# Kernel optimization log

Measured on AMD Instinct MI355X. Metric: run time of the kernel, lower is better.

## Reference

```python
import math
import jax, jax.numpy as jnp
import numpy as np

D = 1536      # d_model
H = 12        # n_heads
L = 12        # n_layers
V = 50257     # vocab (hardcoded in module)
P = 1024      # max positions (hardcoded)
B = 1         # batch (must be 1: pos-embed uses arange(len(idx)))
S = 1024      # sequence length


def setup_inputs() -> dict:
    key = jax.random.key(0)
    ks = jax.random.split(key, 10)
    sc = 0.02
    n = lambda k, shape: (jax.random.normal(k, shape, jnp.float32) * sc)
    return {
        "idx": jax.random.randint(ks[0], (B, S), 0, V),
        "mask": jnp.tril(jnp.ones((S, S), jnp.int32)),  # causal mask
        "tok_emb": n(ks[1], (V, D)),
        "pos_emb": n(ks[2], (P, D)),
        "Wqkv": n(ks[3], (L, D, 3 * D)), "bqkv": jnp.zeros((L, 3 * D), jnp.float32),
        "Wo":   n(ks[4], (L, D, D)),     "bo":   jnp.zeros((L, D), jnp.float32),
        "W1":   n(ks[5], (L, D, 4 * D)), "b1":   jnp.zeros((L, 4 * D), jnp.float32),
        "W2":   n(ks[6], (L, 4 * D, D)), "b2":   jnp.zeros((L, D), jnp.float32),
        "ln_g": jnp.ones((D,), jnp.float32), "ln_b": jnp.zeros((D,), jnp.float32),
        "Wout": n(ks[7], (D, D)), "bout": jnp.zeros((D,), jnp.float32),
    }


def _gpt_forward(idx, mask, tok_emb, pos_emb, Wqkv, bqkv, Wo, bo,
                 W1, b1, W2, b2, ln_g, ln_b, Wout, bout):
    b, s = idx.shape
    d = tok_emb.shape[1]
    hd = d // H
    scale = 1.0 / math.sqrt(d)  # note: module divides by sqrt(d_model), not head_dim

    # faithful quirk: position_embedding(arange(len(idx))) -> (B, D), broadcasts since B==1
    x = tok_emb[idx] + pos_emb[:b]  # (B,S,D)

    mask0 = (mask == 0)  # (S,S) -> broadcast over (B,H,S,S)

    def block(x, p):
        wqkv, bqkv_, wo, bo_, w1, b1_, w2, b2_ = p
        qkv = x @ wqkv + bqkv_                       # (B,S,3D)
        q, k, v = jnp.split(qkv, 3, axis=-1)
        q = q.reshape(b, s, H, hd)
        k = k.reshape(b, s, H, hd)
        v = v.reshape(b, s, H, hd)
        scores = jnp.einsum('bqhd,bkhd->bhqk', q, k) * scale
        scores = jnp.where(mask0, -jnp.inf, scores)
        attn = jax.nn.softmax(scores, axis=-2)       # non-standard: softmax over QUERY axis
        o = jnp.einsum('bhqk,bkhd->bqhd', attn, v).reshape(b, s, d)
        x = x + (o @ wo + bo_)                       # attention residual
        x = x + (jax.nn.relu(x @ w1 + b1_) @ w2 + b2_)  # FFN residual (on post-attn x)
        return x, None

    x, _ = jax.lax.scan(block, x, (Wqkv, bqkv, Wo, bo, W1, b1, W2, b2))

    # final LayerNorm (eps=1e-5 like torch default)
    mu = jnp.mean(x, axis=-1, keepdims=True)
    var = jnp.mean(jnp.square(x - mu), axis=-1, keepdims=True)
    xn = (x - mu) * jax.lax.rsqrt(var + 1e-5) * ln_g + ln_b
    return xn @ Wout + bout


def reference(idx, mask, tok_emb, pos_emb, Wqkv, bqkv, Wo, bo,
              W1, b1, W2, b2, ln_g, ln_b, Wout, bout):
    return _gpt_forward(idx, mask, tok_emb, pos_emb, Wqkv, bqkv, Wo, bo,
                        W1, b1, W2, b2, ln_g, ln_b, Wout, bout)
```

## Files before the change

kernel.cpp:

```cpp
#include <hip/hip_runtime.h>
#include <stdint.h>
#include <math.h>

#define D_MODEL 1536
#define NH 12
#define HD 128
#define NL 12
#define SEQ 1024
#define D3 4608
#define D4 6144
#define SCALE 0.025515518153991442f

typedef __attribute__((ext_vector_type(8))) short short8;
typedef __attribute__((ext_vector_type(4))) float floatx4;

__device__ __forceinline__ uint32_t packhi(float a, float b) {
  return (__float_as_uint(a) >> 16) | (__float_as_uint(b) & 0xFFFF0000u);
}
__device__ __forceinline__ float truncf32(float a) {
  return __uint_as_float(__float_as_uint(a) & 0xFFFF0000u);
}
__device__ __forceinline__ void split8v(float4 v0, float4 v1, uint4 &hi, uint4 &lo) {
  hi.x = packhi(v0.x, v0.y); hi.y = packhi(v0.z, v0.w);
  hi.z = packhi(v1.x, v1.y); hi.w = packhi(v1.z, v1.w);
  lo.x = packhi(v0.x - truncf32(v0.x), v0.y - truncf32(v0.y));
  lo.y = packhi(v0.z - truncf32(v0.z), v0.w - truncf32(v0.w));
  lo.z = packhi(v1.x - truncf32(v1.x), v1.y - truncf32(v1.y));
  lo.w = packhi(v1.z - truncf32(v1.z), v1.w - truncf32(v1.w));
}

__device__ __forceinline__ int xcd_chunk_id(int nwg) {
  int orig = blockIdx.x;
  int xcd = orig & 7, pos = orig >> 3;
  int q = nwg >> 3, r = nwg & 7;
  return (xcd < r ? xcd * (q + 1) : r * (q + 1) + (xcd - r) * q) + pos;
}

__global__ __launch_bounds__(256)
void embed_kernel(const int* __restrict__ idx, const float* __restrict__ tok,
                  const float* __restrict__ pos, float* __restrict__ x) {
  int i = blockIdx.x * 256 + threadIdx.x;
  int s = i / D_MODEL;
  int d = i - s * D_MODEL;
  x[i] = tok[(size_t)idx[s] * D_MODEL + d] + pos[d];
}

template<int BM, bool RELU, bool RES, int SPLITK, bool TA2>
__global__ __launch_bounds__(256)
void mgemm_kernel(const float* __restrict__ A, const float* __restrict__ Ab,
                  const float* __restrict__ B,
                  const float* __restrict__ bias, const float* __restrict__ res,
                  float* __restrict__ C, int M, int N, int K, int NC, int NR) {
  constexpr int MI = BM / 32;
  constexpr int AE = BM / 8;
  constexpr int TPR = 32 / AE;
  __shared__ short Ah[2][BM][36], Al[2][BM][36];
  __shared__ short Bh[2][128][36], Bl[2][128][36];
  const int tid = threadIdx.x;
  const int lane = tid & 63, wave = tid >> 6;

  const int lid = xcd_chunk_id(NC * NR * SPLITK);
  const int z   = lid / (NC * NR);
  const int rem = lid - z * (NC * NR);
  const int ct  = rem / NR;
  const int rt  = rem - ct * NR;
  const int bm = rt * BM, bn = ct << 7;

  const int wm = (wave >> 1) * (BM / 2), wn = (wave & 1) << 6;
  const int fr = lane & 15, fk = (lane >> 4) << 3;
  const int Kc = K / SPLITK;
  const int kbase = (SPLITK > 1) ? z * Kc : 0;

  floatx4 acc[MI][4];
#pragma unroll
  for (int i = 0; i < MI; i++)
#pragma unroll
    for (int j = 0; j < 4; j++) acc[i][j] = (floatx4){0.f, 0.f, 0.f, 0.f};

  const int ar = tid / TPR;
  const int ac = (tid % TPR) * AE;
  const int bc = tid & 127;
  const int bkq = (tid >> 7) << 4;
  const float* Ag  = A + (size_t)(bm + ar) * K + kbase + ac;
  const float* Ag2 = TA2 ? (Ab + (size_t)(bm + ar) * K + kbase + ac) : nullptr;
  const float* Bg = B + (size_t)(kbase + bkq) * N + bn + bc;

  float a_reg[AE];
  float b_reg[16];

  auto LOADG = [&](int k0) {
#pragma unroll
    for (int e = 0; e < AE / 4; e++) {
      float4 v = *(const float4*)(Ag + k0 + 4 * e);
      if constexpr (TA2) {
        float4 w = *(const float4*)(Ag2 + k0 + 4 * e);
        v.x += w.x; v.y += w.y; v.z += w.z; v.w += w.w;
      }
      a_reg[4 * e + 0] = v.x; a_reg[4 * e + 1] = v.y;
      a_reg[4 * e + 2] = v.z; a_reg[4 * e + 3] = v.w;
    }
    const float* Bp = Bg + (size_t)k0 * N;
#pragma unroll
    for (int j = 0; j < 16; j++) b_reg[j] = Bp[(size_t)j * N];
  };
  auto STORE = [&](int buf) {
#pragma unroll
    for (int e = 0; e < AE / 8; e++) {
      float4 v0 = {a_reg[8 * e + 0], a_reg[8 * e + 1], a_reg[8 * e + 2], a_reg[8 * e + 3]};
      float4 v1 = {a_reg[8 * e + 4], a_reg[8 * e + 5], a_reg[8 * e + 6], a_reg[8 * e + 7]};
      uint4 hi, lo; split8v(v0, v1, hi, lo);
      *(uint4*)&Ah[buf][ar][ac + 8 * e] = hi;
      *(uint4*)&Al[buf][ar][ac + 8 * e] = lo;
    }
#pragma unroll
    for (int e = 0; e < 2; e++) {
      float4 u0 = {b_reg[8 * e + 0], b_reg[8 * e + 1], b_reg[8 * e + 2], b_reg[8 * e + 3]};
      float4 u1 = {b_reg[8 * e + 4], b_reg[8 * e + 5], b_reg[8 * e + 6], b_reg[8 * e + 7]};
      uint4 hi, lo; split8v(u0, u1, hi, lo);
      *(uint4*)&Bh[buf][bc][bkq + 8 * e] = hi;
      *(uint4*)&Bl[buf][bc][bkq + 8 * e] = lo;
    }
  };

  LOADG(0);
  STORE(0);
  __syncthreads();

  for (int k0 = 0; k0 < Kc; k0 += 32) {
    const int cur = (k0 >> 5) & 1;
    const bool more = (k0 + 32 < Kc);
    if (more) LOADG(k0 + 32);

    short8 ah[MI], al[MI], bh[4], bl[4];
#pragma unroll
    for (int i = 0; i < MI; i++) {
      ah[i] = *(const short8*)&Ah[cur][wm + (i << 4) + fr][fk];
      al[i] = *(const short8*)&Al[cur][wm + (i << 4) + fr][fk];
    }
#pragma unroll
    for (int j = 0; j < 4; j++) {
      bh[j] = *(const short8*)&Bh[cur][wn + (j << 4) + fr][fk];
      bl[j] = *(const short8*)&Bl[cur][wn + (j << 4) + fr][fk];
    }
#pragma unroll
    for (int i = 0; i < MI; i++)
#pragma unroll
      for (int j = 0; j < 4; j++) {
        acc[i][j] = __builtin_amdgcn_mfma_f32_16x16x32_bf16(ah[i], bh[j], acc[i][j], 0, 0, 0);
        acc[i][j] = __builtin_amdgcn_mfma_f32_16x16x32_bf16(ah[i], bl[j], acc[i][j], 0, 0, 0);
        acc[i][j] = __builtin_amdgcn_mfma_f32_16x16x32_bf16(al[i], bh[j], acc[i][j], 0, 0, 0);
      }

    if (more) STORE(cur ^ 1);
    __syncthreads();
  }

  const int cr = (lane >> 4) << 2, cc = lane & 15;
  if constexpr (SPLITK > 1) {
    float* Cp = C + (size_t)z * M * N;
#pragma unroll
    for (int j = 0; j < 4; j++) {
      const int col = bn + wn + (j << 4) + cc;
#pragma unroll
      for (int i = 0; i < MI; i++) {
        const int row0 = bm + wm + (i << 4) + cr;
#pragma unroll
        for (int r = 0; r < 4; r++)
          Cp[(size_t)(row0 + r) * N + col] = acc[i][j][r];
      }
    }
  } else {
#pragma unroll
    for (int j = 0; j < 4; j++) {
      const int col = bn + wn + (j << 4) + cc;
      const float bv = bias[col];
#pragma unroll
      for (int i = 0; i < MI; i++) {
        const int row0 = bm + wm + (i << 4) + cr;
#pragma unroll
        for (int r = 0; r < 4; r++) {
          float v = acc[i][j][r] + bv;
          if constexpr (RES) v += res[(size_t)(row0 + r) * N + col];
          if constexpr (RELU) v = fmaxf(v, 0.f);
          C[(size_t)(row0 + r) * N + col] = v;
        }
      }
    }
  }
}

template<bool HASB, bool RES, bool RELU>
__global__ __launch_bounds__(256)
void combine_kernel(const float* __restrict__ p0, const float* __restrict__ p1,
                    const float* __restrict__ bias, const float* __restrict__ res,
                    float* __restrict__ C, int N) {
  const int i = (blockIdx.x * 256 + threadIdx.x) << 2;
  float4 a = *(const float4*)&p0[i];
  float4 b = *(const float4*)&p1[i];
  float4 r = {a.x + b.x, a.y + b.y, a.z + b.z, a.w + b.w};
  if constexpr (HASB) {
    const int col = i % N;
    float4 bv = *(const float4*)&bias[col];
    r.x += bv.x; r.y += bv.y; r.z += bv.z; r.w += bv.w;
  }
  if constexpr (RES) {
    float4 rv = *(const float4*)&res[i];
    r.x += rv.x; r.y += rv.y; r.z += rv.z; r.w += rv.w;
  }
  if constexpr (RELU) {
    r.x = fmaxf(r.x, 0.f); r.y = fmaxf(r.y, 0.f);
    r.z = fmaxf(r.z, 0.f); r.w = fmaxf(r.w, 0.f);
  }
  *(float4*)&C[i] = r;
}

__global__ __launch_bounds__(256)
void scores_kernel(const float* __restrict__ qkv, float* __restrict__ scores,
                   float* __restrict__ pstats) {
  __shared__ short Qh[128][40], Ql[128][40], Kh[128][40], Kl[128][40];
  const int tid = threadIdx.x;
  const int lane = tid & 63, wave = tid >> 6;

  const int lid = xcd_chunk_id(NH * 36);
  const int h = lid / 36;
  int t = lid - h * 36;
  int rr = 0;
  while ((rr + 1) * (rr + 2) / 2 <= t) rr++;
  const int bi = rr << 7;
  const int bj = (t - rr * (rr + 1) / 2) << 7;

  const int wm = (wave >> 1) << 6, wn = (wave & 1) << 6;
  const int fr = lane & 15, fk = (lane >> 4) << 3;
  const float* Q = qkv + h * HD;
  const float* Kp = qkv + D_MODEL + h * HD;

  floatx4 acc[4][4];
#pragma unroll
  for (int i = 0; i < 4; i++)
#pragma unroll
    for (int j = 0; j < 4; j++) acc[i][j] = (floatx4){0.f, 0.f, 0.f, 0.f};

  const int ar = tid >> 1;
  const int ac = (tid & 1) << 4;

  for (int k0 = 0; k0 < HD; k0 += 32) {
    __syncthreads();
    {
      const float* Qp = Q + (size_t)(bi + ar) * D3 + k0 + ac;
#pragma unroll
      for (int e = 0; e < 2; e++) {
        float4 v0 = *(const float4*)(Qp + 8 * e);
        float4 v1 = *(const float4*)(Qp + 8 * e + 4);
        uint4 hi, lo; split8v(v0, v1, hi, lo);
        *(uint4*)&Qh[ar][ac + 8 * e] = hi;
        *(uint4*)&Ql[ar][ac + 8 * e] = lo;
      }
      const float* Kpp = Kp + (size_t)(bj + ar) * D3 + k0 + ac;
#pragma unroll
      for (int e = 0; e < 2; e++) {
        float4 v0 = *(const float4*)(Kpp + 8 * e);
        float4 v1 = *(const float4*)(Kpp + 8 * e + 4);
        uint4 hi, lo; split8v(v0, v1, hi, lo);
        *(uint4*)&Kh[ar][ac + 8 * e] = hi;
        *(uint4*)&Kl[ar][ac + 8 * e] = lo;
      }
    }
    __syncthreads();
    short8 qh[4], ql[4], kh[4], kl[4];
#pragma unroll
    for (int i = 0; i < 4; i++) {
      qh[i] = *(const short8*)&Qh[wm + (i << 4) + fr][fk];
      ql[i] = *(const short8*)&Ql[wm + (i << 4) + fr][fk];
      kh[i] = *(const short8*)&Kh[wn + (i << 4) + fr][fk];
      kl[i] = *(const short8*)&Kl[wn + (i << 4) + fr][fk];
    }
#pragma unroll
    for (int i = 0; i < 4; i++)
#pragma unroll
      for (int j = 0; j < 4; j++) {
        acc[i][j] = __builtin_amdgcn_mfma_f32_16x16x32_bf16(qh[i], kh[j], acc[i][j], 0, 0, 0);
        acc[i][j] = __builtin_amdgcn_mfma_f32_16x16x32_bf16(qh[i], kl[j], acc[i][j], 0, 0, 0);
        acc[i][j] = __builtin_amdgcn_mfma_f32_16x16x32_bf16(ql[i], kh[j], acc[i][j], 0, 0, 0);
        acc[i][j] = __builtin_amdgcn_mfma_f32_16x16x32_bf16(ql[i], kl[j], acc[i][j], 0, 0, 0);
      }
  }

  const int cr = (lane >> 4) << 2, cc = lane & 15;
  float* S = scores + (size_t)h * SEQ * SEQ;
  const int qc = (bi >> 6) + (wave >> 1);
  float* Pm = pstats + (size_t)((h * 16 + qc) * 2 + 0) * 1024;
  float* Pz = pstats + (size_t)((h * 16 + qc) * 2 + 1) * 1024;
#pragma unroll
  for (int j = 0; j < 4; j++) {
    const int col = bj + wn + (j << 4) + cc;
    float vv[16];
    float m = -1e30f;
#pragma unroll
    for (int i = 0; i < 4; i++) {
      const int row0 = bi + wm + (i << 4) + cr;
#pragma unroll
      for (int r = 0; r < 4; r++) {
        float v = (col <= row0 + r) ? acc[i][j][r] * SCALE : -1e30f;
        S[(size_t)(row0 + r) * SEQ + col] = v;
        vv[i * 4 + r] = v;
        m = fmaxf(m, v);
      }
    }
    float zz = 0.f;
#pragma unroll
    for (int t2 = 0; t2 < 16; t2++) zz += __expf(vv[t2] - m);
    if (m == -1e30f) zz = 0.f;
#pragma unroll
    for (int off = 16; off <= 32; off <<= 1) {
      float mo = __shfl_xor(m, off, 64);
      float zo = __shfl_xor(zz, off, 64);
      float mn = fmaxf(m, mo);
      zz = zz * __expf(m - mn) + zo * __expf(mo - mn);
      m = mn;
    }
    if ((lane >> 4) == 0) { Pm[col] = m; Pz[col] = zz; }
  }
}

__global__ __launch_bounds__(256)
void av_kernel(const float* __restrict__ qkv, const float* __restrict__ scores,
               const float* __restrict__ pstats, float* __restrict__ part) {
  __shared__ short Ph[64][40], Pl[64][40], Vh[128][40], Vl[128][40];
  __shared__ float Ms[512], Rs[512];
  const int tid = threadIdx.x;
  const int lane = tid & 63, wave = tid >> 6;

  const int lid = xcd_chunk_id(NH * 32);
  const int h = lid >> 5;
  const int t = lid & 31;
  const int y = t >> 1, z = t & 1;
  const int bm = y << 6;

  const int wm = (wave >> 1) << 5, wn = (wave & 1) << 6;
  const int fr = lane & 15, fk = (lane >> 4) << 3;
  const float* S = scores + (size_t)h * SEQ * SEQ;
  const float* V = qkv + 2 * D_MODEL + h * HD;

  const int kbeg = z * (y + 1) * 32;
  const int kend = (z + 1) * (y + 1) * 32;
  const int ncols = kend - kbeg;

  for (int c0 = tid; c0 < ncols; c0 += 256) {
    const int c = kbeg + c0;
    const int q0 = c >> 6;
    float m = -1e30f;
    for (int qc = q0; qc < 16; qc++)
      m = fmaxf(m, pstats[(size_t)((h * 16 + qc) * 2 + 0) * 1024 + c]);
    float zz = 0.f;
    for (int qc = q0; qc < 16; qc++) {
      float pm = pstats[(size_t)((h * 16 + qc) * 2 + 0) * 1024 + c];
      float pz = pstats[(size_t)((h * 16 + qc) * 2 + 1) * 1024 + c];
      zz += pz * __expf(pm - m);
    }
    Ms[c0] = m;
    Rs[c0] = 1.f / zz;
  }

  floatx4 acc[2][4];
#pragma unroll
  for (int i = 0; i < 2; i++)
#pragma unroll
    for (int j = 0; j < 4; j++) acc[i][j] = (floatx4){0.f, 0.f, 0.f, 0.f};

  const int ar = tid >> 2;
  const int ac = (tid & 3) << 3;
  const int bc = tid & 127;
  const int bkq = (tid >> 7) << 4;

  for (int k0 = kbeg; k0 < kend; k0 += 32) {
    __syncthreads();
    {
      const float* Sp = S + (size_t)(bm + ar) * SEQ + k0 + ac;
      float4 v0 = *(const float4*)(Sp);
      float4 v1 = *(const float4*)(Sp + 4);
      float t8[8] = {v0.x, v0.y, v0.z, v0.w, v1.x, v1.y, v1.z, v1.w};
      float4 p0, p1;
      {
        int kk = k0 - kbeg + ac;
        p0.x = __expf(t8[0] - Ms[kk + 0]) * Rs[kk + 0];
        p0.y = __expf(t8[1] - Ms[kk + 1]) * Rs[kk + 1];
        p0.z = __expf(t8[2] - Ms[kk + 2]) * Rs[kk + 2];
        p0.w = __expf(t8[3] - Ms[kk + 3]) * Rs[kk + 3];
        p1.x = __expf(t8[4] - Ms[kk + 4]) * Rs[kk + 4];
        p1.y = __expf(t8[5] - Ms[kk + 5]) * Rs[kk + 5];
        p1.z = __expf(t8[6] - Ms[kk + 6]) * Rs[kk + 6];
        p1.w = __expf(t8[7] - Ms[kk + 7]) * Rs[kk + 7];
      }
      uint4 hi, lo; split8v(p0, p1, hi, lo);
      *(uint4*)&Ph[ar][ac] = hi;
      *(uint4*)&Pl[ar][ac] = lo;
    }
    {
      const float* Vp = V + (size_t)(k0 + bkq) * D3 + bc;
#pragma unroll
      for (int e = 0; e < 2; e++) {
        float4 u0, u1;
        u0.x = Vp[(size_t)(8 * e + 0) * D3]; u0.y = Vp[(size_t)(8 * e + 1) * D3];
        u0.z = Vp[(size_t)(8 * e + 2) * D3]; u0.w = Vp[(size_t)(8 * e + 3) * D3];
        u1.x = Vp[(size_t)(8 * e + 4) * D3]; u1.y = Vp[(size_t)(8 * e + 5) * D3];
        u1.z = Vp[(size_t)(8 * e + 6) * D3]; u1.w = Vp[(size_t)(8 * e + 7) * D3];
        uint4 hi, lo; split8v(u0, u1, hi, lo);
        *(uint4*)&Vh[bc][bkq + 8 * e] = hi;
        *(uint4*)&Vl[bc][bkq + 8 * e] = lo;
      }
    }
    __syncthreads();
    short8 ph[2], pl[2], vh[4], vl[4];
#pragma unroll
    for (int i = 0; i < 2; i++) {
      ph[i] = *(const short8*)&Ph[wm + (i << 4) + fr][fk];
      pl[i] = *(const short8*)&Pl[wm + (i << 4) + fr][fk];
    }
#pragma unroll
    for (int j = 0; j < 4; j++) {
      vh[j] = *(const short8*)&Vh[wn + (j << 4) + fr][fk];
      vl[j] = *(const short8*)&Vl[wn + (j << 4) + fr][fk];
    }
#pragma unroll
    for (int i = 0; i < 2; i++)
#pragma unroll
      for (int j = 0; j < 4; j++) {
        acc[i][j] = __builtin_amdgcn_mfma_f32_16x16x32_bf16(ph[i], vh[j], acc[i][j], 0, 0, 0);
        acc[i][j] = __builtin_amdgcn_mfma_f32_16x16x32_bf16(ph[i], vl[j], acc[i][j], 0, 0, 0);
        acc[i][j] = __builtin_amdgcn_mfma_f32_16x16x32_bf16(pl[i], vh[j], acc[i][j], 0, 0, 0);
      }
  }

  const int cr = (lane >> 4) << 2, cc = lane & 15;
  float* Cp = part + (size_t)z * SEQ * D_MODEL;
#pragma unroll
  for (int j = 0; j < 4; j++) {
    const int col = h * HD + wn + (j << 4) + cc;
#pragma unroll
    for (int i = 0; i < 2; i++) {
      const int row0 = bm + wm + (i << 4) + cr;
#pragma unroll
      for (int r = 0; r < 4; r++)
        Cp[(size_t)(row0 + r) * D_MODEL + col] = acc[i][j][r];
    }
  }
}

__global__ __launch_bounds__(256)
void ln_kernel(const float* __restrict__ x, const float* __restrict__ g,
               const float* __restrict__ bb, float* __restrict__ y) {
  __shared__ float red[8];
  const int row = blockIdx.x;
  const float* xr = x + (size_t)row * D_MODEL;
  float v[6];
  float s = 0.f, sq = 0.f;
#pragma unroll
  for (int i = 0; i < 6; i++) {
    v[i] = xr[256 * i + threadIdx.x];
    s += v[i];
    sq += v[i] * v[i];
  }
#pragma unroll
  for (int off = 32; off >= 1; off >>= 1) {
    s += __shfl_down(s, off, 64);
    sq += __shfl_down(sq, off, 64);
  }
  const int lane = threadIdx.x & 63, w = threadIdx.x >> 6;
  if (lane == 0) { red[w] = s; red[4 + w] = sq; }
  __syncthreads();
  if (threadIdx.x == 0) {
    red[0] = red[0] + red[1] + red[2] + red[3];
    red[4] = red[4] + red[5] + red[6] + red[7];
  }
  __syncthreads();
  const float mu = red[0] * (1.f / D_MODEL);
  const float var = red[4] * (1.f / D_MODEL) - mu * mu;
  const float rs = rsqrtf(var + 1e-5f);
#pragma unroll
  for (int i = 0; i < 6; i++) {
    int c = 256 * i + threadIdx.x;
    y[(size_t)row * D_MODEL + c] = (v[i] - mu) * rs * g[c] + bb[c];
  }
}

extern "C" void kernel_launch(void* const* d_in, const int* in_sizes, int n_in,
                              void* d_out, int out_size, void* d_ws, size_t ws_size,
                              hipStream_t stream) {
  (void)in_sizes; (void)n_in; (void)out_size; (void)ws_size;
  const int*   idx     = (const int*)d_in[0];
  const float* tok_emb = (const float*)d_in[2];
  const float* pos_emb = (const float*)d_in[3];
  const float* Wqkv    = (const float*)d_in[4];
  const float* bqkv    = (const float*)d_in[5];
  const float* Wo      = (const float*)d_in[6];
  const float* bo      = (const float*)d_in[7];
  const float* W1      = (const float*)d_in[8];
  const float* b1      = (const float*)d_in[9];
  const float* W2      = (const float*)d_in[10];
  const float* b2      = (const float*)d_in[11];
  const float* ln_g    = (const float*)d_in[12];
  const float* ln_b    = (const float*)d_in[13];
  const float* Wout    = (const float*)d_in[14];
  const float* bout    = (const float*)d_in[15];
  float* out = (float*)d_out;

  char* ws = (char*)d_ws;
  float* x      = (float*)(ws);
  float* qkv    = (float*)(ws + 6291456);
  float* pstats = (float*)(ws + 25165824);
  float* part   = (float*)(ws + 26836992);
  float* U      = (float*)(ws + 52002816);
  float* scores = U;
  float* h1     = U;
  float* xn     = U;
  const size_t PN = (size_t)SEQ * D_MODEL;

  embed_kernel<<<6144, 256, 0, stream>>>(idx, tok_emb, pos_emb, x);

  for (int l = 0; l < NL; l++) {
    const float* wqkv = Wqkv + (size_t)l * D_MODEL * D3;
    const float* bq   = bqkv + (size_t)l * D3;
    const float* wo   = Wo   + (size_t)l * D_MODEL * D_MODEL;
    const float* bo_  = bo   + (size_t)l * D_MODEL;
    const float* w1   = W1   + (size_t)l * D_MODEL * D4;
    const float* b1_  = b1   + (size_t)l * D4;
    const float* w2   = W2   + (size_t)l * D4 * D_MODEL;
    const float* b2_  = b2   + (size_t)l * D_MODEL;

    mgemm_kernel<128, false, false, 1, false><<<288, 256, 0, stream>>>(
        x, nullptr, wqkv, bq, nullptr, qkv, SEQ, D3, D_MODEL, 36, 8);
    scores_kernel<<<432, 256, 0, stream>>>(qkv, scores, pstats);
    av_kernel<<<384, 256, 0, stream>>>(qkv, scores, pstats, part);
    mgemm_kernel<64, false, false, 2, true><<<384, 256, 0, stream>>>(
        part, part + PN, wo, nullptr, nullptr, part + 2 * PN,
        SEQ, D_MODEL, D_MODEL, 12, 16);
    combine_kernel<true, true, false><<<1536, 256, 0, stream>>>(
        part + 2 * PN, part + 3 * PN, bo_, x, x, D_MODEL);
    mgemm_kernel<128, true, false, 1, false><<<384, 256, 0, stream>>>(
        x, nullptr, w1, b1_, nullptr, h1, SEQ, D4, D_MODEL, 48, 8);
    mgemm_kernel<64, false, false, 2, false><<<384, 256, 0, stream>>>(
        h1, nullptr, w2, nullptr, nullptr, part, SEQ, D_MODEL, D4, 12, 16);
    combine_kernel<true, true, false><<<1536, 256, 0, stream>>>(
        part, part + PN, b2_, x, x, D_MODEL);
  }

  ln_kernel<<<SEQ, 256, 0, stream>>>(x, ln_g, ln_b, xn);
  mgemm_kernel<64, false, false, 2, false><<<384, 256, 0, stream>>>(
      xn, nullptr, Wout, nullptr, nullptr, part, SEQ, D_MODEL, D_MODEL, 12, 16);
  combine_kernel<true, false, false><<<1536, 256, 0, stream>>>(
      part, part + PN, bout, nullptr, out, D_MODEL);
}
```

Measured before the change: 5.060 ms.

## Fuse whole forward pass into a persistent cooperative megakernel with grid syncs

Replaces roughly a hundred separate kernel launches with one cooperative persistent kernel that loops over work items for each stage and uses grid-wide syncs between stages. The goal is to remove launch overhead and inter-kernel gaps. To fit a shared smem buffer and two blocks per CU, the GEMM drops its register/LDS double buffering and syncs twice per k-step, which may cost GEMM throughput. Fixed grid size (up to 768 blocks) means stages with more work items than blocks run in multiple passes. A fallback path keeps the old multi-kernel sequence.

```diff
diff --git a/kernel.cpp b/kernel.cpp
--- a/kernel.cpp
+++ b/kernel.cpp
@@ -1,6 +1,9 @@
 #include <hip/hip_runtime.h>
+#include <hip/hip_cooperative_groups.h>
 #include <stdint.h>
 #include <math.h>
+
+namespace cg = cooperative_groups;
 
 #define D_MODEL 1536
 #define NH 12
@@ -29,37 +32,39 @@
   lo.w = packhi(v1.z - truncf32(v1.z), v1.w - truncf32(v1.w));
 }
 
-__device__ __forceinline__ int xcd_chunk_id(int nwg) {
-  int orig = blockIdx.x;
+__device__ __forceinline__ int xcd_chunk(int orig, int nwg) {
   int xcd = orig & 7, pos = orig >> 3;
   int q = nwg >> 3, r = nwg & 7;
   return (xcd < r ? xcd * (q + 1) : r * (q + 1) + (xcd - r) * q) + pos;
 }
 
-__global__ __launch_bounds__(256)
-void embed_kernel(const int* __restrict__ idx, const float* __restrict__ tok,
-                  const float* __restrict__ pos, float* __restrict__ x) {
-  int i = blockIdx.x * 256 + threadIdx.x;
+__device__ __forceinline__ void d_embed(int wi, const int* __restrict__ idx,
+                                        const float* __restrict__ tok,
+                                        const float* __restrict__ pos,
+                                        float* __restrict__ x) {
+  int i = wi * 256 + threadIdx.x;
   int s = i / D_MODEL;
   int d = i - s * D_MODEL;
   x[i] = tok[(size_t)idx[s] * D_MODEL + d] + pos[d];
 }
 
 template<int BM, bool RELU, bool RES, int SPLITK, bool TA2>
-__global__ __launch_bounds__(256)
-void mgemm_kernel(const float* __restrict__ A, const float* __restrict__ Ab,
-                  const float* __restrict__ B,
-                  const float* __restrict__ bias, const float* __restrict__ res,
-                  float* __restrict__ C, int M, int N, int K, int NC, int NR) {
+__device__ void d_mgemm(char* smem, int orig,
+                        const float* __restrict__ A, const float* __restrict__ Ab,
+                        const float* __restrict__ B,
+                        const float* __restrict__ bias, const float* __restrict__ res,
+                        float* __restrict__ C, int M, int N, int K, int NC, int NR) {
   constexpr int MI = BM / 32;
   constexpr int AE = BM / 8;
   constexpr int TPR = 32 / AE;
-  __shared__ short Ah[2][BM][36], Al[2][BM][36];
-  __shared__ short Bh[2][128][36], Bl[2][128][36];
+  short* AhS = (short*)smem;
+  short* AlS = AhS + BM * 36;
+  short* BhS = AlS + BM * 36;
+  short* BlS = BhS + 128 * 36;
   const int tid = threadIdx.x;
   const int lane = tid & 63, wave = tid >> 6;
 
-  const int lid = xcd_chunk_id(NC * NR * SPLITK);
+  const int lid = xcd_chunk(orig, NC * NR * SPLITK);
   const int z   = lid / (NC * NR);
   const int rem = lid - z * (NC * NR);
   const int ct  = rem / NR;
@@ -88,7 +93,7 @@
   float a_reg[AE];
   float b_reg[16];
 
-  auto LOADG = [&](int k0) {
+  for (int k0 = 0; k0 < Kc; k0 += 32) {
 #pragma unroll
     for (int e = 0; e < AE / 4; e++) {
       float4 v = *(const float4*)(Ag + k0 + 4 * e);
@@ -99,48 +104,40 @@
       a_reg[4 * e + 0] = v.x; a_reg[4 * e + 1] = v.y;
       a_reg[4 * e + 2] = v.z; a_reg[4 * e + 3] = v.w;
     }
-    const float* Bp = Bg + (size_t)k0 * N;
-#pragma unroll
-    for (int j = 0; j < 16; j++) b_reg[j] = Bp[(size_t)j * N];
-  };
-  auto STORE = [&](int buf) {
+    {
+      const float* Bp = Bg + (size_t)k0 * N;
+#pragma unroll
+      for (int j = 0; j < 16; j++) b_reg[j] = Bp[(size_t)j * N];
+    }
+    __syncthreads();
 #pragma unroll
     for (int e = 0; e < AE / 8; e++) {
       float4 v0 = {a_reg[8 * e + 0], a_reg[8 * e + 1], a_reg[8 * e + 2], a_reg[8 * e + 3]};
       float4 v1 = {a_reg[8 * e + 4], a_reg[8 * e + 5], a_reg[8 * e + 6], a_reg[8 * e + 7]};
       uint4 hi, lo; split8v(v0, v1, hi, lo);
-      *(uint4*)&Ah[buf][ar][ac + 8 * e] = hi;
-      *(uint4*)&Al[buf][ar][ac + 8 * e] = lo;
+      *(uint4*)&AhS[ar * 36 + ac + 8 * e] = hi;
+      *(uint4*)&AlS[ar * 36 + ac + 8 * e] = lo;
     }
 #pragma unroll
     for (int e = 0; e < 2; e++) {
       float4 u0 = {b_reg[8 * e + 0], b_reg[8 * e + 1], b_reg[8 * e + 2], b_reg[8 * e + 3]};
       float4 u1 = {b_reg[8 * e + 4], b_reg[8 * e + 5], b_reg[8 * e + 6], b_reg[8 * e + 7]};
       uint4 hi, lo; split8v(u0, u1, hi, lo);
-      *(uint4*)&Bh[buf][bc][bkq + 8 * e] = hi;
-      *(uint4*)&Bl[buf][bc][bkq + 8 * e] = lo;
-    }
-  };
-
-  LOADG(0);
-  STORE(0);
-  __syncthreads();
-
-  for (int k0 = 0; k0 < Kc; k0 += 32) {
-    const int cur = (k0 >> 5) & 1;
-    const bool more = (k0 + 32 < Kc);
-    if (more) LOADG(k0 + 32);
+      *(uint4*)&BhS[bc * 36 + bkq + 8 * e] = hi;
+      *(uint4*)&BlS[bc * 36 + bkq + 8 * e] = lo;
+    }
+    __syncthreads();
 
     short8 ah[MI], al[MI], bh[4], bl[4];
 #pragma unroll
     for (int i = 0; i < MI; i++) {
-      ah[i] = *(const short8*)&Ah[cur][wm + (i << 4) + fr][fk];
-      al[i] = *(const short8*)&Al[cur][wm + (i << 4) + fr][fk];
+      ah[i] = *(const short8*)&AhS[(wm + (i << 4) + fr) * 36 + fk];
+      al[i] = *(const short8*)&AlS[(wm + (i << 4) + fr) * 36 + fk];
     }
 #pragma unroll
     for (int j = 0; j < 4; j++) {
-      bh[j] = *(const short8*)&Bh[cur][wn + (j << 4) + fr][fk];
-      bl[j] = *(const short8*)&Bl[cur][wn + (j << 4) + fr][fk];
+      bh[j] = *(const short8*)&BhS[(wn + (j << 4) + fr) * 36 + fk];
+      bl[j] = *(const short8*)&BlS[(wn + (j << 4) + fr) * 36 + fk];
     }
 #pragma unroll
     for (int i = 0; i < MI; i++)
@@ -150,10 +147,8 @@
         acc[i][j] = __builtin_amdgcn_mfma_f32_16x16x32_bf16(ah[i], bl[j], acc[i][j], 0, 0, 0);
         acc[i][j] = __builtin_amdgcn_mfma_f32_16x16x32_bf16(al[i], bh[j], acc[i][j], 0, 0, 0);
       }
-
-    if (more) STORE(cur ^ 1);
-    __syncthreads();
-  }
+  }
+  __syncthreads();
 
   const int cr = (lane >> 4) << 2, cc = lane & 15;
   if constexpr (SPLITK > 1) {
@@ -189,39 +184,16 @@
   }
 }
 
-template<bool HASB, bool RES, bool RELU>
-__global__ __launch_bounds__(256)
-void combine_kernel(const float* __restrict__ p0, const float* __restrict__ p1,
-                    const float* __restrict__ bias, const float* __restrict__ res,
-                    float* __restrict__ C, int N) {
-  const int i = (blockIdx.x * 256 + threadIdx.x) << 2;
-  float4 a = *(const float4*)&p0[i];
-  float4 b = *(const float4*)&p1[i];
-  float4 r = {a.x + b.x, a.y + b.y, a.z + b.z, a.w + b.w};
-  if constexpr (HASB) {
-    const int col = i % N;
-    float4 bv = *(const float4*)&bias[col];
-    r.x += bv.x; r.y += bv.y; r.z += bv.z; r.w += bv.w;
-  }
-  if constexpr (RES) {
-    float4 rv = *(const float4*)&res[i];
-    r.x += rv.x; r.y += rv.y; r.z += rv.z; r.w += rv.w;
-  }
-  if constexpr (RELU) {
-    r.x = fmaxf(r.x, 0.f); r.y = fmaxf(r.y, 0.f);
-    r.z = fmaxf(r.z, 0.f); r.w = fmaxf(r.w, 0.f);
-  }
-  *(float4*)&C[i] = r;
-}
-
-__global__ __launch_bounds__(256)
-void scores_kernel(const float* __restrict__ qkv, float* __restrict__ scores,
-                   float* __restrict__ pstats) {
-  __shared__ short Qh[128][40], Ql[128][40], Kh[128][40], Kl[128][40];
+__device__ void d_scores(char* smem, int orig, const float* __restrict__ qkv,
+                         float* __restrict__ scores, float* __restrict__ pstats) {
+  short* QhS = (short*)smem;
+  short* QlS = QhS + 5120;
+  short* KhS = QlS + 5120;
+  short* KlS = KhS + 5120;
   const int tid = threadIdx.x;
   const int lane = tid & 63, wave = tid >> 6;
 
-  const int lid = xcd_chunk_id(NH * 36);
+  const int lid = xcd_chunk(orig, NH * 36);
   const int h = lid / 36;
   int t = lid - h * 36;
   int rr = 0;
@@ -252,8 +224,8 @@
         float4 v0 = *(const float4*)(Qp + 8 * e);
         float4 v1 = *(const float4*)(Qp + 8 * e + 4);
         uint4 hi, lo; split8v(v0, v1, hi, lo);
-        *(uint4*)&Qh[ar][ac + 8 * e] = hi;
-        *(uint4*)&Ql[ar][ac + 8 * e] = lo;
+        *(uint4*)&QhS[ar * 40 + ac + 8 * e] = hi;
+        *(uint4*)&QlS[ar * 40 + ac + 8 * e] = lo;
       }
       const float* Kpp = Kp + (size_t)(bj + ar) * D3 + k0 + ac;
 #pragma unroll
@@ -261,18 +233,18 @@
         float4 v0 = *(const float4*)(Kpp + 8 * e);
         float4 v1 = *(const float4*)(Kpp + 8 * e + 4);
         uint4 hi, lo; split8v(v0, v1, hi, lo);
-        *(uint4*)&Kh[ar][ac + 8 * e] = hi;
-        *(uint4*)&Kl[ar][ac + 8 * e] = lo;
+        *(uint4*)&KhS[ar * 40 + ac + 8 * e] = hi;
+        *(uint4*)&KlS[ar * 40 + ac + 8 * e] = lo;
       }
     }
     __syncthreads();
     short8 qh[4], ql[4], kh[4], kl[4];
 #pragma unroll
     for (int i = 0; i < 4; i++) {
-      qh[i] = *(const short8*)&Qh[wm + (i << 4) + fr][fk];
-      ql[i] = *(const short8*)&Ql[wm + (i << 4) + fr][fk];
-      kh[i] = *(const short8*)&Kh[wn + (i << 4) + fr][fk];
-      kl[i] = *(const short8*)&Kl[wn + (i << 4) + fr][fk];
+      qh[i] = *(const short8*)&QhS[(wm + (i << 4) + fr) * 40 + fk];
+      ql[i] = *(const short8*)&QlS[(wm + (i << 4) + fr) * 40 + fk];
+      kh[i] = *(const short8*)&KhS[(wn + (i << 4) + fr) * 40 + fk];
+      kl[i] = *(const short8*)&KlS[(wn + (i << 4) + fr) * 40 + fk];
     }
 #pragma unroll
     for (int i = 0; i < 4; i++)
@@ -284,6 +256,7 @@
         acc[i][j] = __builtin_amdgcn_mfma_f32_16x16x32_bf16(ql[i], kl[j], acc[i][j], 0, 0, 0);
       }
   }
+  __syncthreads();
 
   const int cr = (lane >> 4) << 2, cc = lane & 15;
   float* S = scores + (size_t)h * SEQ * SEQ;
@@ -322,15 +295,19 @@
   }
 }
 
-__global__ __launch_bounds__(256)
-void av_kernel(const float* __restrict__ qkv, const float* __restrict__ scores,
-               const float* __restrict__ pstats, float* __restrict__ part) {
-  __shared__ short Ph[64][40], Pl[64][40], Vh[128][40], Vl[128][40];
-  __shared__ float Ms[512], Rs[512];
+__device__ void d_av(char* smem, int orig, const float* __restrict__ qkv,
+                     const float* __restrict__ scores, const float* __restrict__ pstats,
+                     float* __restrict__ part) {
+  short* PhS = (short*)smem;
+  short* PlS = PhS + 2560;
+  short* VhS = PlS + 2560;
+  short* VlS = VhS + 5120;
+  float* Ms = (float*)(smem + 30720);
+  float* Rs = Ms + 512;
   const int tid = threadIdx.x;
   const int lane = tid & 63, wave = tid >> 6;
 
-  const int lid = xcd_chunk_id(NH * 32);
+  const int lid = xcd_chunk(orig, NH * 32);
   const int h = lid >> 5;
   const int t = lid & 31;
   const int y = t >> 1, z = t & 1;
@@ -345,6 +322,7 @@
   const int kend = (z + 1) * (y + 1) * 32;
   const int ncols = kend - kbeg;
 
+  __syncthreads();
   for (int c0 = tid; c0 < ncols; c0 += 256) {
     const int c = kbeg + c0;
     const int q0 = c >> 6;
@@ -392,8 +370,8 @@
         p1.w = __expf(t8[7] - Ms[kk + 7]) * Rs[kk + 7];
       }
       uint4 hi, lo; split8v(p0, p1, hi, lo);
-      *(uint4*)&Ph[ar][ac] = hi;
-      *(uint4*)&Pl[ar][ac] = lo;
+      *(uint4*)&PhS[ar * 40 + ac] = hi;
+      *(uint4*)&PlS[ar * 40 + ac] = lo;
     }
     {
       const float* Vp = V + (size_t)(k0 + bkq) * D3 + bc;
@@ -405,21 +383,21 @@
         u1.x = Vp[(size_t)(8 * e + 4) * D3]; u1.y = Vp[(size_t)(8 * e + 5) * D3];
         u1.z = Vp[(size_t)(8 * e + 6) * D3]; u1.w = Vp[(size_t)(8 * e + 7) * D3];
         uint4 hi, lo; split8v(u0, u1, hi, lo);
-        *(uint4*)&Vh[bc][bkq + 8 * e] = hi;
-        *(uint4*)&Vl[bc][bkq + 8 * e] = lo;
+        *(uint4*)&VhS[bc * 40 + bkq + 8 * e] = hi;
+        *(uint4*)&VlS[bc * 40 + bkq + 8 * e] = lo;
       }
     }
     __syncthreads();
     short8 ph[2], pl[2], vh[4], vl[4];
 #pragma unroll
     for (int i = 0; i < 2; i++) {
-      ph[i] = *(const short8*)&Ph[wm + (i << 4) + fr][fk];
-      pl[i] = *(const short8*)&Pl[wm + (i << 4) + fr][fk];
+      ph[i] = *(const short8*)&PhS[(wm + (i << 4) + fr) * 40 + fk];
+      pl[i] = *(const short8*)&PlS[(wm + (i << 4) + fr) * 40 + fk];
     }
 #pragma unroll
     for (int j = 0; j < 4; j++) {
-      vh[j] = *(const short8*)&Vh[wn + (j << 4) + fr][fk];
-      vl[j] = *(const short8*)&Vl[wn + (j << 4) + fr][fk];
+      vh[j] = *(const short8*)&VhS[(wn + (j << 4) + fr) * 40 + fk];
+      vl[j] = *(const short8*)&VlS[(wn + (j << 4) + fr) * 40 + fk];
     }
 #pragma unroll
     for (int i = 0; i < 2; i++)
@@ -430,6 +408,7 @@
         acc[i][j] = __builtin_amdgcn_mfma_f32_16x16x32_bf16(pl[i], vh[j], acc[i][j], 0, 0, 0);
       }
   }
+  __syncthreads();
 
   const int cr = (lane >> 4) << 2, cc = lane & 15;
   float* Cp = part + (size_t)z * SEQ * D_MODEL;
@@ -446,11 +425,36 @@
   }
 }
 
-__global__ __launch_bounds__(256)
-void ln_kernel(const float* __restrict__ x, const float* __restrict__ g,
-               const float* __restrict__ bb, float* __restrict__ y) {
-  __shared__ float red[8];
-  const int row = blockIdx.x;
+template<bool HASB, bool RES, bool RELU>
+__device__ __forceinline__ void d_combine(int wi, const float* __restrict__ p0,
+                                          const float* __restrict__ p1,
+                                          const float* __restrict__ bias,
+                                          const float* __restrict__ res,
+                                          float* __restrict__ C, int N) {
+  const int i = (wi * 256 + threadIdx.x) << 2;
+  float4 a = *(const float4*)&p0[i];
+  float4 b = *(const float4*)&p1[i];
+  float4 r = {a.x + b.x, a.y + b.y, a.z + b.z, a.w + b.w};
+  if constexpr (HASB) {
+    const int col = i % N;
+    float4 bv = *(const float4*)&bias[col];
+    r.x += bv.x; r.y += bv.y; r.z += bv.z; r.w += bv.w;
+  }
+  if constexpr (RES) {
+    float4 rv = *(const float4*)&res[i];
+    r.x += rv.x; r.y += rv.y; r.z += rv.z; r.w += rv.w;
+  }
+  if constexpr (RELU) {
+    r.x = fmaxf(r.x, 0.f); r.y = fmaxf(r.y, 0.f);
+    r.z = fmaxf(r.z, 0.f); r.w = fmaxf(r.w, 0.f);
+  }
+  *(float4*)&C[i] = r;
+}
+
+__device__ void d_ln(char* smem, int row, const float* __restrict__ x,
+                     const float* __restrict__ g, const float* __restrict__ bb,
+                     float* __restrict__ y) {
+  float* red = (float*)smem;
   const float* xr = x + (size_t)row * D_MODEL;
   float v[6];
   float s = 0.f, sq = 0.f;
@@ -466,6 +470,7 @@
     sq += __shfl_down(sq, off, 64);
   }
   const int lane = threadIdx.x & 63, w = threadIdx.x >> 6;
+  __syncthreads();
   if (lane == 0) { red[w] = s; red[4 + w] = sq; }
   __syncthreads();
   if (threadIdx.x == 0) {
@@ -481,72 +486,208 @@
     int c = 256 * i + threadIdx.x;
     y[(size_t)row * D_MODEL + c] = (v[i] - mu) * rs * g[c] + bb[c];
   }
+  __syncthreads();
+}
+
+struct Params {
+  const int* idx;
+  const float* tok_emb; const float* pos_emb;
+  const float* Wqkv; const float* bqkv;
+  const float* Wo; const float* bo;
+  const float* W1; const float* b1;
+  const float* W2; const float* b2;
+  const float* ln_g; const float* ln_b;
+  const float* Wout; const float* bout;
+  float* out;
+  float* x; float* qkv; float* pstats; float* part;
+  float* scores; float* h1; float* xn;
+};
+
+__global__ __launch_bounds__(256, 2)
+void gpt_mega(Params p) {
+  cg::grid_group grid = cg::this_grid();
+  __shared__ __align__(16) char smem[40960];
+  const int bid = blockIdx.x;
+  const int gsz = gridDim.x;
+  const size_t PN = (size_t)SEQ * D_MODEL;
+
+  for (int wi = bid; wi < 6144; wi += gsz)
+    d_embed(wi, p.idx, p.tok_emb, p.pos_emb, p.x);
+  grid.sync();
+
+  for (int l = 0; l < NL; l++) {
+    const float* wqkv = p.Wqkv + (size_t)l * D_MODEL * D3;
+    const float* bq   = p.bqkv + (size_t)l * D3;
+    const float* wo   = p.Wo   + (size_t)l * D_MODEL * D_MODEL;
+    const float* bo_  = p.bo   + (size_t)l * D_MODEL;
+    const float* w1   = p.W1   + (size_t)l * D_MODEL * D4;
+    const float* b1_  = p.b1   + (size_t)l * D4;
+    const float* w2   = p.W2   + (size_t)l * D4 * D_MODEL;
+    const float* b2_  = p.b2   + (size_t)l * D_MODEL;
+
+    for (int wi = bid; wi < 288; wi += gsz)
+      d_mgemm<128, false, false, 1, false>(smem, wi, p.x, nullptr, wqkv, bq, nullptr,
+                                           p.qkv, SEQ, D3, D_MODEL, 36, 8);
+    grid.sync();
+    for (int wi = bid; wi < 432; wi += gsz)
+      d_scores(smem, wi, p.qkv, p.scores, p.pstats);
+    grid.sync();
+    for (int wi = bid; wi < 384; wi += gsz)
+      d_av(smem, wi, p.qkv, p.scores, p.pstats, p.part);
+    grid.sync();
+    for (int wi = bid; wi < 384; wi += gsz)
+      d_mgemm<64, false, false, 2, true>(smem, wi, p.part, p.part + PN, wo, nullptr,
+                                         nullptr, p.part + 2 * PN, SEQ, D_MODEL,
+                                         D_MODEL, 12, 16);
+    grid.sync();
+    for (int wi = bid; wi < 1536; wi += gsz)
+      d_combine<true, true, false>(wi, p.part + 2 * PN, p.part + 3 * PN, bo_, p.x,
+                                   p.x, D_MODEL);
+    grid.sync();
+    for (int wi = bid; wi < 384; wi += gsz)
+      d_mgemm<128, true, false, 1, false>(smem, wi, p.x, nullptr, w1, b1_, nullptr,
+                                          p.h1, SEQ, D4, D_MODEL, 48, 8);
+    grid.sync();
+    for (int wi = bid; wi < 384; wi += gsz)
+      d_mgemm<64, false, false, 2, false>(smem, wi, p.h1, nullptr, w2, nullptr,
+                                          nullptr, p.part, SEQ, D_MODEL, D4, 12, 16);
+    grid.sync();
+    for (int wi = bid; wi < 1536; wi += gsz)
+      d_combine<true, true, false>(wi, p.part, p.part + PN, b2_, p.x, p.x, D_MODEL);
+    grid.sync();
+  }
+
+  for (int wi = bid; wi < SEQ; wi += gsz)
+    d_ln(smem, wi, p.x, p.ln_g, p.ln_b, p.xn);
+  grid.sync();
+  for (int wi = bid; wi < 384; wi += gsz)
+    d_mgemm<64, false, false, 2, false>(smem, wi, p.xn, nullptr, p.Wout, nullptr,
+                                        nullptr, p.part, SEQ, D_MODEL, D_MODEL, 12, 16);
+  grid.sync();
+  for (int wi = bid; wi < 1536; wi += gsz)
+    d_combine<true, false, false>(wi, p.part, p.part + PN, p.bout, nullptr, p.out,
+                                  D_MODEL);
+}
+
+__global__ __launch_bounds__(256)
+void w_embed(Params p) { d_embed(blockIdx.x, p.idx, p.tok_emb, p.pos_emb, p.x); }
+
+template<int BM, bool RELU, bool RES, int SPLITK, bool TA2>
+__global__ __launch_bounds__(256)
+void w_mgemm(const float* A, const float* Ab, const float* B, const float* bias,
+             const float* res, float* C, int M, int N, int K, int NC, int NR) {
+  __shared__ __align__(16) char smem[36864];
+  d_mgemm<BM, RELU, RES, SPLITK, TA2>(smem, blockIdx.x, A, Ab, B, bias, res, C,
+                                      M, N, K, NC, NR);
+}
+
+__global__ __launch_bounds__(256)
+void w_scores(const float* qkv, float* scores, float* pstats) {
+  __shared__ __align__(16) char smem[40960];
+  d_scores(smem, blockIdx.x, qkv, scores, pstats);
+}
+
+__global__ __launch_bounds__(256)
+void w_av(const float* qkv, const float* scores, const float* pstats, float* part) {
+  __shared__ __align__(16) char smem[34816];
+  d_av(smem, blockIdx.x, qkv, scores, pstats, part);
+}
+
+template<bool HASB, bool RES, bool RELU>
+__global__ __launch_bounds__(256)
+void w_combine(const float* p0, const float* p1, const float* bias, const float* res,
+               float* C, int N) {
+  d_combine<HASB, RES, RELU>(blockIdx.x, p0, p1, bias, res, C, N);
+}
+
+__global__ __launch_bounds__(256)
+void w_ln(const float* x, const float* g, const float* bb, float* y) {
+  __shared__ __align__(16) char smem[64];
+  d_ln(smem, blockIdx.x, x, g, bb, y);
 }
 
 extern "C" void kernel_launch(void* const* d_in, const int* in_sizes, int n_in,
                               void* d_out, int out_size, void* d_ws, size_t ws_size,
                               hipStream_t stream) {
   (void)in_sizes; (void)n_in; (void)out_size; (void)ws_size;
-  const int*   idx     = (const int*)d_in[0];
-  const float* tok_emb = (const float*)d_in[2];
-  const float* pos_emb = (const float*)d_in[3];
-  const float* Wqkv    = (const float*)d_in[4];
-  const float* bqkv    = (const float*)d_in[5];
-  const float* Wo      = (const float*)d_in[6];
-  const float* bo      = (const float*)d_in[7];
-  const float* W1      = (const float*)d_in[8];
-  const float* b1      = (const float*)d_in[9];
-  const float* W2      = (const float*)d_in[10];
-  const float* b2      = (const float*)d_in[11];
-  const float* ln_g    = (const float*)d_in[12];
-  const float* ln_b    = (const float*)d_in[13];
-  const float* Wout    = (const float*)d_in[14];
-  const float* bout    = (const float*)d_in[15];
-  float* out = (float*)d_out;
-
   char* ws = (char*)d_ws;
-  float* x      = (float*)(ws);
-  float* qkv    = (float*)(ws + 6291456);
-  float* pstats = (float*)(ws + 25165824);
-  float* part   = (float*)(ws + 26836992);
-  float* U      = (float*)(ws + 52002816);
-  float* scores = U;
-  float* h1     = U;
-  float* xn     = U;
+  Params p;
+  p.idx     = (const int*)d_in[0];
+  p.tok_emb = (const float*)d_in[2];
+  p.pos_emb = (const float*)d_in[3];
+  p.Wqkv    = (const float*)d_in[4];
+  p.bqkv    = (const float*)d_in[5];
+  p.Wo      = (const float*)d_in[6];
+  p.bo      = (const float*)d_in[7];
+  p.W1      = (const float*)d_in[8];
+  p.b1      = (const float*)d_in[9];
+  p.W2      = (const float*)d_in[10];
+  p.b2      = (const float*)d_in[11];
+  p.ln_g    = (const float*)d_in[12];
+  p.ln_b    = (const float*)d_in[13];
+  p.Wout    = (const float*)d_in[14];
+  p.bout    = (const float*)d_in[15];
+  p.out     = (float*)d_out;
+  p.x      = (float*)(ws);
+  p.qkv    = (float*)(ws + 6291456);
+  p.pstats = (float*)(ws + 25165824);
+  p.part   = (float*)(ws + 26836992);
+  p.scores = (float*)(ws + 52002816);
+  p.h1     = p.scores;
+  p.xn     = p.scores;
+
+  int nCU = 0;
+  {
+    hipDeviceProp_t prop;
+    int dev = 0;
+    if (hipGetDevice(&dev) == hipSuccess &&
+        hipGetDeviceProperties(&prop, dev) == hipSuccess)
+      nCU = prop.multiProcessorCount;
+  }
+  int perCU = 0;
+  hipError_t occ = hipOccupancyMaxActiveBlocksPerMultiprocessor(&perCU, gpt_mega, 256, 0);
+  bool launched = false;
+  if (occ == hipSuccess && nCU > 0 && perCU > 0) {
+    int gridSz = perCU * nCU;
+    if (gridSz > 768) gridSz = 768;
+    void* args[] = {&p};
+    hipError_t e = hipLaunchCooperativeKernel((void*)gpt_mega, dim3(gridSz),
+                                              dim3(256), args, 0, stream);
+    if (e == hipSuccess) launched = true;
+  }
+  if (launched) return;
+
   const size_t PN = (size_t)SEQ * D_MODEL;
-
-  embed_kernel<<<6144, 256, 0, stream>>>(idx, tok_emb, pos_emb, x);
-
+  w_embed<<<6144, 256, 0, stream>>>(p);
   for (int l = 0; l < NL; l++) {
-    const float* wqkv = Wqkv + (size_t)l * D_MODEL * D3;
-    const float* bq   = bqkv + (size_t)l * D3;
-    const float* wo   = Wo   + (size_t)l * D_MODEL * D_MODEL;
-    const float* bo_  = bo   + (size_t)l * D_MODEL;
-    const float* w1   = W1   + (size_t)l * D_MODEL * D4;
-    const float* b1_  = b1   + (size_t)l * D4;
-    const float* w2   = W2   + (size_t)l * D4 * D_MODEL;
-    const float* b2_  = b2   + (size_t)l * D_MODEL;
-
-    mgemm_kernel<128, false, false, 1, false><<<288, 256, 0, stream>>>(
-        x, nullptr, wqkv, bq, nullptr, qkv, SEQ, D3, D_MODEL, 36, 8);
-    scores_kernel<<<432, 256, 0, stream>>>(qkv, scores, pstats);
-    av_kernel<<<384, 256, 0, stream>>>(qkv, scores, pstats, part);
-    mgemm_kernel<64, false, false, 2, true><<<384, 256, 0, stream>>>(
-        part, part + PN, wo, nullptr, nullptr, part + 2 * PN,
+    const float* wqkv = p.Wqkv + (size_t)l * D_MODEL * D3;
+    const float* bq   = p.bqkv + (size_t)l * D3;
+    const float* wo   = p.Wo   + (size_t)l * D_MODEL * D_MODEL;
+    const float* bo_  = p.bo   + (size_t)l * D_MODEL;
+    const float* w1   = p.W1   + (size_t)l * D_MODEL * D4;
+    const float* b1_  = p.b1   + (size_t)l * D4;
+    const float* w2   = p.W2   + (size_t)l * D4 * D_MODEL;
+    const float* b2_  = p.b2   + (size_t)l * D_MODEL;
+
+    w_mgemm<128, false, false, 1, false><<<288, 256, 0, stream>>>(
+        p.x, nullptr, wqkv, bq, nullptr, p.qkv, SEQ, D3, D_MODEL, 36, 8);
+    w_scores<<<432, 256, 0, stream>>>(p.qkv, p.scores, p.pstats);
+    w_av<<<384, 256, 0, stream>>>(p.qkv, p.scores, p.pstats, p.part);
+    w_mgemm<64, false, false, 2, true><<<384, 256, 0, stream>>>(
+        p.part, p.part + PN, wo, nullptr, nullptr, p.part + 2 * PN,
         SEQ, D_MODEL, D_MODEL, 12, 16);
-    combine_kernel<true, true, false><<<1536, 256, 0, stream>>>(
-        part + 2 * PN, part + 3 * PN, bo_, x, x, D_MODEL);
-    mgemm_kernel<128, true, false, 1, false><<<384, 256, 0, stream>>>(
-        x, nullptr, w1, b1_, nullptr, h1, SEQ, D4, D_MODEL, 48, 8);
-    mgemm_kernel<64, false, false, 2, false><<<384, 256, 0, stream>>>(
-        h1, nullptr, w2, nullptr, nullptr, part, SEQ, D_MODEL, D4, 12, 16);
-    combine_kernel<true, true, false><<<1536, 256, 0, stream>>>(
-        part, part + PN, b2_, x, x, D_MODEL);
-  }
-
-  ln_kernel<<<SEQ, 256, 0, stream>>>(x, ln_g, ln_b, xn);
-  mgemm_kernel<64, false, false, 2, false><<<384, 256, 0, stream>>>(
-      xn, nullptr, Wout, nullptr, nullptr, part, SEQ, D_MODEL, D_MODEL, 12, 16);
-  combine_kernel<true, false, false><<<1536, 256, 0, stream>>>(
-      part, part + PN, bout, nullptr, out, D_MODEL);
-}
+    w_combine<true, true, false><<<1536, 256, 0, stream>>>(
+        p.part + 2 * PN, p.part + 3 * PN, bo_, p.x, p.x, D_MODEL);
+    w_mgemm<128, true, false, 1, false><<<384, 256, 0, stream>>>(
+        p.x, nullptr, w1, b1_, nullptr, p.h1, SEQ, D4, D_MODEL, 48, 8);
+    w_mgemm<64, false, false, 2, false><<<384, 256, 0, stream>>>(
+        p.h1, nullptr, w2, nullptr, nullptr, p.part, SEQ, D_MODEL, D4, 12, 16);
+    w_combine<true, true, false><<<1536, 256, 0, stream>>>(
+        p.part, p.part + PN, b2_, p.x, p.x, D_MODEL);
+  }
+  w_ln<<<SEQ, 256, 0, stream>>>(p.x, p.ln_g, p.ln_b, p.xn);
+  w_mgemm<64, false, false, 2, false><<<384, 256, 0, stream>>>(
+      p.xn, nullptr, p.Wout, nullptr, nullptr, p.part, SEQ, D_MODEL, D_MODEL, 12, 16);
+  w_combine<true, false, false><<<1536, 256, 0, stream>>>(
+      p.part, p.part + PN, p.bout, nullptr, p.out, D_MODEL);
+}
```

Measured after the change: 13.73 ms. 2.71x slower.
